# Optimization experiments

Hardware: AMD Instinct MI355X
Metric: run time of the kernel (lower is better)

## Reference

```python
import jax, jax.numpy as jnp
import numpy as np

N = 4096
IN_DIM = 256
HID = 64
HEADS = 4
OUT_DIM = 64
NEG = -9e15


def setup_inputs() -> dict:
    key = jax.random.key(0)
    ks = jax.random.split(key, 12)
    h = jax.random.normal(ks[0], (N, IN_DIM), dtype=jnp.float32)
    adj = jax.random.randint(ks[1], (N, N), 0, 2, dtype=jnp.int32)
    # per-head GATLayer params (W: Linear(input_dim, hid) with bias; a: Linear(2*hid, 1) with bias)
    Wh = jax.random.normal(ks[2], (HEADS, IN_DIM, HID), dtype=jnp.float32) * (1.414 / np.sqrt(IN_DIM + HID))
    bWh = jnp.zeros((HEADS, HID), dtype=jnp.float32)
    a_src = jax.random.normal(ks[3], (HEADS, HID), dtype=jnp.float32) * 0.1
    a_dst = jax.random.normal(ks[4], (HEADS, HID), dtype=jnp.float32) * 0.1
    a_b = jnp.zeros((HEADS,), dtype=jnp.float32)
    # output GATLayer params
    Wo = jax.random.normal(ks[5], (HEADS * HID, OUT_DIM), dtype=jnp.float32) * (1.414 / np.sqrt(HEADS * HID + OUT_DIM))
    bWo = jnp.zeros((OUT_DIM,), dtype=jnp.float32)
    ao_src = jax.random.normal(ks[6], (OUT_DIM,), dtype=jnp.float32) * 0.1
    ao_dst = jax.random.normal(ks[7], (OUT_DIM,), dtype=jnp.float32) * 0.1
    ao_b = jnp.zeros((), dtype=jnp.float32)
    return {"h": h, "adj": adj, "Wh": Wh, "bWh": bWh, "a_src": a_src, "a_dst": a_dst,
            "a_b": a_b, "Wo": Wo, "bWo": bWo, "ao_src": ao_src, "ao_dst": ao_dst, "ao_b": ao_b}


def _gat_layer(x, adj_mask, W, b, a_s, a_d, a_bias):
    # x: [N, F], W: [F, D]. Decompose a([wh_i || wh_j]) = a_s.wh_i + a_d.wh_j + a_bias
    wh = x @ W + b                                   # [N, D]
    s = (wh @ a_s)[:, None] + (wh @ a_d)[None, :] + a_bias  # [N, N]
    s = jax.nn.leaky_relu(s, negative_slope=0.2)
    s = jnp.where(adj_mask, s, NEG)
    att = jax.nn.softmax(s, axis=1)                  # softmax over neighbors j
    return att @ wh                                  # [N, D]


def reference(h, adj, Wh, bWh, a_src, a_dst, a_b, Wo, bWo, ao_src, ao_dst, ao_b):
    adj_mask = adj > 0
    # multi-head: vmap over stacked head params (dropout is identity in eval)
    heads = jax.vmap(lambda W, b, asr, ads, ab: _gat_layer(h, adj_mask, W, b, asr, ads, ab))(
        Wh, bWh, a_src, a_dst, a_b)                  # [H, N, D]
    out = jax.nn.elu(heads)
    out = jnp.transpose(out, (1, 0, 2)).reshape(N, HEADS * HID)  # concat heads
    out = _gat_layer(out, adj_mask, Wo, bWo, ao_src, ao_dst, ao_b)
    return jax.nn.elu(out)
```

## Files before the change

### kernel.cpp

```cpp
#include <hip/hip_runtime.h>

#define NN 4096
#define NHEADS 4
#define HID 64
#define INDIM 256

using short8 = __attribute__((ext_vector_type(8))) short;
using f32x4  = __attribute__((ext_vector_type(4))) float;

union f32u { float f; unsigned int u; };
union i4s8 { int4 i; short8 s; };

__device__ __forceinline__ float bf2f(unsigned short s) {
  f32u x; x.u = ((unsigned int)s) << 16; return x.f;
}
__device__ __forceinline__ unsigned short f2bf(float f) {
  f32u x; x.f = f;
  unsigned int r = x.u + 0x7fffu + ((x.u >> 16) & 1u);
  return (unsigned short)(r >> 16);
}
__device__ __forceinline__ unsigned int cvtpk(float lo, float hi) {
  unsigned int r;
  asm("v_cvt_pk_bf16_f32 %0, %1, %2" : "=v"(r) : "v"(lo), "v"(hi));
  return r;
}

__device__ __forceinline__ float ld(const unsigned short* p, size_t i) { return bf2f(p[i]); }
__device__ __forceinline__ float ld(const float* p, size_t i) { return p[i]; }
__device__ __forceinline__ void ld4(const unsigned short* p, float* out) {
  short4 v = *(const short4*)p;
  out[0] = bf2f((unsigned short)v.x); out[1] = bf2f((unsigned short)v.y);
  out[2] = bf2f((unsigned short)v.z); out[3] = bf2f((unsigned short)v.w);
}
__device__ __forceinline__ void ld4(const float* p, float* out) {
  float4 a = *(const float4*)p;
  out[0] = a.x; out[1] = a.y; out[2] = a.z; out[3] = a.w;
}

__global__ __launch_bounds__(256) void k_bm(const void* adjv, const void* hv,
                                            int* __restrict__ flags,
                                            unsigned char* __restrict__ bm) {
  __shared__ int s_at;
  const int tid = threadIdx.x;
  if (tid == 0) s_at = 0;
  __syncthreads();
  const unsigned int* au = (const unsigned int*)adjv;
  unsigned int wv = au[tid];
  if ((wv & 0xFFFFu) == 0x3F80u) atomicOr(&s_at, 2);
  else if (wv == 0x3F800000u) atomicOr(&s_at, 1);
  __syncthreads();
  const int at = (s_at & 2) ? 2 : (s_at & 1);
  const int i = blockIdx.x;
  if (i == 0 && tid < 64) {
    const unsigned short* hu = (const unsigned short*)hv;
    int bad = 0;
    for (int t = tid; t < 256; t += 64) {
      float v = bf2f(hu[t]);
      if (!(v > -1000.f && v < 1000.f)) bad = 1;
    }
    unsigned long long m = __ballot(bad);
    if (tid == 0) { flags[0] = m ? 0 : 1; flags[1] = at; }
  }
#pragma unroll
  for (int rep = 0; rep < 2; rep++) {
    int jb = tid + rep * 256;
    unsigned int b = 0;
    if (at == 0) {
      const int4* arow = (const int4*)((const int*)adjv + (size_t)i * NN);
      int4 a0 = arow[jb * 2 + 0];
      int4 a1 = arow[jb * 2 + 1];
      b |= (a0.x > 0) ? 1u : 0u;  b |= (a0.y > 0) ? 2u : 0u;
      b |= (a0.z > 0) ? 4u : 0u;  b |= (a0.w > 0) ? 8u : 0u;
      b |= (a1.x > 0) ? 16u : 0u; b |= (a1.y > 0) ? 32u : 0u;
      b |= (a1.z > 0) ? 64u : 0u; b |= (a1.w > 0) ? 128u : 0u;
    } else if (at == 1) {
      const float* arow = (const float*)adjv + (size_t)i * NN + jb * 8;
      for (int t = 0; t < 8; t++) b |= (arow[t] > 0.5f) ? (1u << t) : 0u;
    } else {
      const unsigned short* arow = (const unsigned short*)adjv + (size_t)i * NN + jb * 8;
      for (int t = 0; t < 8; t++) b |= (bf2f(arow[t]) > 0.5f) ? (1u << t) : 0u;
    }
    bm[(size_t)i * 512 + jb] = (unsigned char)b;
  }
}

template <typename T>
__device__ __forceinline__ void wh_body(const T* h, const T* Wh, const T* bWh,
    const T* a_src, const T* a_dst, const T* a_b,
    unsigned short* __restrict__ Bp1, float* __restrict__ ssrc1, float* __restrict__ sdst1,
    float (*hs)[260], float (*wp)[16][260], float* av0, float* av1) {
  const int tid = threadIdx.x;
  const int w = tid >> 6, lane = tid & 63;
  const int head = w & 3, kq = w >> 2;
  const int rb = blockIdx.x;
  const int R0 = rb * 16;
  const int d = lane;
  {
    const int r = tid >> 6, c4 = (tid & 63) * 4;
    float hv4[4];
    ld4(h + (size_t)(R0 + r) * 256 + c4, hv4);
    hs[r][c4 + 0] = hv4[0]; hs[r][c4 + 1] = hv4[1];
    hs[r][c4 + 2] = hv4[2]; hs[r][c4 + 3] = hv4[3];
  }
  if (tid < 256) av0[tid] = ld(a_src, tid);
  else if (tid < 512) av1[tid - 256] = ld(a_dst, tid - 256);
  __syncthreads();
  float acc[16];
  float bv = (kq == 0) ? ld(bWh, head * 64 + d) : 0.f;
#pragma unroll
  for (int r = 0; r < 16; r++) acc[r] = bv;
  const int k0 = kq * 64;
  for (int kb = 0; kb < 8; kb++) {
    float wv[8];
#pragma unroll
    for (int j = 0; j < 8; j++)
      wv[j] = ld(Wh, (size_t)(head * 256 + k0 + kb * 8 + j) * 64 + d);
#pragma unroll
    for (int r = 0; r < 16; r++) {
      float4 ha = *(const float4*)(&hs[r][k0 + kb * 8]);
      float4 hb = *(const float4*)(&hs[r][k0 + kb * 8 + 4]);
      acc[r] = fmaf(ha.x, wv[0], acc[r]);
      acc[r] = fmaf(ha.y, wv[1], acc[r]);
      acc[r] = fmaf(ha.z, wv[2], acc[r]);
      acc[r] = fmaf(ha.w, wv[3], acc[r]);
      acc[r] = fmaf(hb.x, wv[4], acc[r]);
      acc[r] = fmaf(hb.y, wv[5], acc[r]);
      acc[r] = fmaf(hb.z, wv[6], acc[r]);
      acc[r] = fmaf(hb.w, wv[7], acc[r]);
    }
  }
  if (kq >= 2) {
#pragma unroll
    for (int r = 0; r < 16; r++) wp[kq - 2][r][head * 64 + d] = acc[r];
  }
  __syncthreads();
  if (kq < 2) {
#pragma unroll
    for (int r = 0; r < 16; r++) wp[kq][r][head * 64 + d] += acc[r];
  }
  __syncthreads();
  if (tid < 512) {
    const int hh = tid >> 7, tt = (tid >> 5) & 3, lnh = tid & 31;
    const int q2 = (rb & 1) * 2 + (lnh >> 4);
    const int ln = q2 * 16 + (lnh & 15);
    const int dd = tt * 16 + (lnh & 15);
    const int rbase = (lnh >> 4) * 8;
    float v[8];
#pragma unroll
    for (int jj = 0; jj < 8; jj++)
      v[jj] = wp[0][rbase + jj][hh * 64 + dd] + wp[1][rbase + jj][hh * 64 + dd];
    i4s8 s;
    s.i.x = cvtpk(v[0], v[1]); s.i.y = cvtpk(v[2], v[3]);
    s.i.z = cvtpk(v[4], v[5]); s.i.w = cvtpk(v[6], v[7]);
    const int kb = rb >> 1;
    *(int4*)(Bp1 + ((((size_t)hh * 128 + kb) * 4 + tt) * 64 + ln) * 8) = s.i;
  } else if (tid < 576) {
    const int t2 = tid - 512;
    const int hh = t2 >> 4, r = t2 & 15;
    float ps = 0.f, pd = 0.f;
    for (int c = 0; c < 64; c++) {
      float wv2 = wp[0][r][hh * 64 + c] + wp[1][r][hh * 64 + c];
      ps = fmaf(wv2, av0[hh * 64 + c], ps);
      pd = fmaf(wv2, av1[hh * 64 + c], pd);
    }
    ssrc1[hh * NN + R0 + r] = ps + ld(a_b, hh);
    sdst1[hh * NN + R0 + r] = pd;
  }
}
__global__ __launch_bounds__(1024, 4) void k_wh(const void* h, const void* Wh, const void* bWh,
    const void* a_src, const void* a_dst, const void* a_b, const int* __restrict__ flags,
    unsigned short* Bp1, float* ssrc1, float* sdst1) {
  __shared__ float hs[16][260];
  __shared__ float wp[2][16][260];
  __shared__ float av0[256], av1[256];
  if (flags[0])
    wh_body<unsigned short>((const unsigned short*)h, (const unsigned short*)Wh,
        (const unsigned short*)bWh, (const unsigned short*)a_src,
        (const unsigned short*)a_dst, (const unsigned short*)a_b, Bp1, ssrc1, sdst1,
        hs, wp, av0, av1);
  else
    wh_body<float>((const float*)h, (const float*)Wh, (const float*)bWh, (const float*)a_src,
        (const float*)a_dst, (const float*)a_b, Bp1, ssrc1, sdst1, hs, wp, av0, av1);
}

__global__ __launch_bounds__(1024, 4) void k_att1s(
    const unsigned char* __restrict__ bm, const float* __restrict__ ssrc,
    const float* __restrict__ sdst, const short8* __restrict__ Bp,
    float* __restrict__ part, float* __restrict__ partl) {
  const int rb = blockIdx.x & 127;
  const int half = blockIdx.x >> 7;
  const int tid = threadIdx.x;
  const int w = tid >> 6;
  const int head = w & 3;
  const int sl = w >> 2;
  const int lane = tid & 63;
  const int r15 = lane & 15, quad = lane >> 4;
  const int row0 = rb * 32 + r15;
  const int row1 = row0 + 16;
  const float si0 = ssrc[head * NN + row0];
  const float si1 = ssrc[head * NN + row1];
  const unsigned char* bmr0 = bm + (size_t)row0 * 512;
  const unsigned char* bmr1 = bm + (size_t)row1 * 512;
  const float* sd = sdst + head * NN;
  const short8* Bh = Bp + (size_t)head * 128 * 4 * 64;
  f32x4 acc0[4], acc1[4];
#pragma unroll
  for (int t = 0; t < 4; t++) { acc0[t] = (f32x4){0,0,0,0}; acc1[t] = (f32x4){0,0,0,0}; }
  float ls0 = 0.f, ls1 = 0.f;
  const int kb0 = half * 64 + sl * 16;
  for (int g = 0; g < 4; g++) {
    const int kbg = kb0 + g * 4;
    int4 u0 = *(const int4*)(bmr0 + kbg * 4);
    int4 u1 = *(const int4*)(bmr1 + kbg * 4);
    int wd0[4] = {u0.x, u0.y, u0.z, u0.w};
    int wd1[4] = {u1.x, u1.y, u1.z, u1.w};
#pragma unroll
    for (int kk = 0; kk < 4; kk++) {
      const int kb = kbg + kk;
      const int j0 = kb * 32 + quad * 8;
      float4 q0 = *(const float4*)(sd + j0);
      float4 q1 = *(const float4*)(sd + j0 + 4);
      float sdv[8] = {q0.x, q0.y, q0.z, q0.w, q1.x, q1.y, q1.z, q1.w};
      unsigned int bits0 = (((unsigned int)wd0[kk]) >> (quad * 8)) & 0xffu;
      unsigned int bits1 = (((unsigned int)wd1[kk]) >> (quad * 8)) & 0xffu;
      float pe0[8], pe1[8];
#pragma unroll
      for (int jj = 0; jj < 8; jj++) {
        float t0 = si0 + sdv[jj];
        float e0 = __expf(fmaxf(t0, 0.2f * t0));
        pe0[jj] = ((bits0 >> jj) & 1u) ? e0 : 0.f;
        ls0 += pe0[jj];
        float t1 = si1 + sdv[jj];
        float e1 = __expf(fmaxf(t1, 0.2f * t1));
        pe1[jj] = ((bits1 >> jj) & 1u) ? e1 : 0.f;
        ls1 += pe1[jj];
      }
      i4s8 a0, a1;
      a0.i.x = cvtpk(pe0[0], pe0[1]); a0.i.y = cvtpk(pe0[2], pe0[3]);
      a0.i.z = cvtpk(pe0[4], pe0[5]); a0.i.w = cvtpk(pe0[6], pe0[7]);
      a1.i.x = cvtpk(pe1[0], pe1[1]); a1.i.y = cvtpk(pe1[2], pe1[3]);
      a1.i.z = cvtpk(pe1[4], pe1[5]); a1.i.w = cvtpk(pe1[6], pe1[7]);
      const short8* Bk = Bh + (size_t)kb * 256 + lane;
      short8 bt[4];
      bt[0] = Bk[0]; bt[1] = Bk[64]; bt[2] = Bk[128]; bt[3] = Bk[192];
#pragma unroll
      for (int t = 0; t < 4; t++) {
        acc0[t] = __builtin_amdgcn_mfma_f32_16x16x32_bf16(a0.s, bt[t], acc0[t], 0, 0, 0);
        acc1[t] = __builtin_amdgcn_mfma_f32_16x16x32_bf16(a1.s, bt[t], acc1[t], 0, 0, 0);
      }
    }
  }
  ls0 += __shfl_xor(ls0, 16); ls0 += __shfl_xor(ls0, 32);
  ls1 += __shfl_xor(ls1, 16); ls1 += __shfl_xor(ls1, 32);
  __shared__ float accs[8][16][66];
  __shared__ float lsh[8][16];
#define DOPASS(AC, LSV, PASS)                                                  \
  do {                                                                         \
    if (sl >= 2) {                                                             \
      const int slot = head * 2 + (sl - 2);                                    \
      if (lane < 16) lsh[slot][lane] = (LSV);                                  \
      _Pragma("unroll") for (int t = 0; t < 4; t++)                            \
        _Pragma("unroll") for (int gg = 0; gg < 4; gg++)                       \
          accs[slot][quad * 4 + gg][t * 16 + r15] = (AC)[t][gg];               \
    }                                                                          \
    __syncthreads();                                                           \
    if (sl < 2) {                                                              \
      const int slot = head * 2 + sl;                                          \
      if (lane < 16) lsh[slot][lane] += (LSV);                                 \
      _Pragma("unroll") for (int t = 0; t < 4; t++)                            \
        _Pragma("unroll") for (int gg = 0; gg < 4; gg++)                       \
          accs[slot][quad * 4 + gg][t * 16 + r15] += (AC)[t][gg];              \
    }                                                                          \
    __syncthreads();                                                           \
    _Pragma("unroll") for (int idx = tid; idx < 4096; idx += 1024) {           \
      int r = idx >> 8, hc = idx & 255;                                        \
      int hh = hc >> 6, col = hc & 63;                                         \
      part[((size_t)half * NN + rb * 32 + (PASS) * 16 + r) * 256 + hc] =       \
          accs[hh * 2][r][col] + accs[hh * 2 + 1][r][col];                     \
    }                                                                          \
    if (tid < 64)                                                              \
      partl[((size_t)half * 4 + (tid >> 4)) * NN + rb * 32 + (PASS) * 16 +     \
            (tid & 15)] = lsh[(tid >> 4) * 2][tid & 15] +                      \
                          lsh[(tid >> 4) * 2 + 1][tid & 15];                   \
    __syncthreads();                                                           \
  } while (0)
  DOPASS(acc0, ls0, 0);
  DOPASS(acc1, ls1, 1);
#undef DOPASS
}

__global__ __launch_bounds__(1024) void k_att1(
    const unsigned char* __restrict__ bm, const float* __restrict__ ssrc,
    const float* __restrict__ sdst, const short8* __restrict__ Bp,
    unsigned short* __restrict__ x2) {
  const int rb = blockIdx.x;
  const int tid = threadIdx.x;
  const int w = tid >> 6;
  const int head = w & 3;
  const int slice = w >> 2;
  const int lane = tid & 63;
  const int r15 = lane & 15, quad = lane >> 4;
  const int row = rb * 16 + r15;
  const float si = ssrc[head * NN + row];
  const unsigned char* bmrow = bm + (size_t)row * 512;
  const float* sd = sdst + head * NN;
  const short8* Bh = Bp + (size_t)head * 128 * 4 * 64;
  f32x4 acc0 = {0, 0, 0, 0}, acc1 = {0, 0, 0, 0}, acc2 = {0, 0, 0, 0}, acc3 = {0, 0, 0, 0};
  float lsum = 0.f;
  const int kb0 = slice * 32;
  for (int kb = kb0; kb < kb0 + 32; kb++) {
    const int j0 = kb * 32 + quad * 8;
    unsigned int bits = bmrow[kb * 4 + quad];
    float4 q0 = *(const float4*)(sd + j0);
    float4 q1 = *(const float4*)(sd + j0 + 4);
    float sdv[8] = {q0.x, q0.y, q0.z, q0.w, q1.x, q1.y, q1.z, q1.w};
    short8 af;
#pragma unroll
    for (int jj = 0; jj < 8; jj++) {
      float t = si + sdv[jj];
      float lr = fmaxf(t, 0.2f * t);
      float e = __expf(lr);
      float pe = ((bits >> jj) & 1u) ? e : 0.0f;
      lsum += pe;
      af[jj] = (short)f2bf(pe);
    }
    const short8* Bk = Bh + (size_t)kb * 256 + lane;
    short8 b0 = Bk[0], b1 = Bk[64], b2 = Bk[128], b3 = Bk[192];
    acc0 = __builtin_amdgcn_mfma_f32_16x16x32_bf16(af, b0, acc0, 0, 0, 0);
    acc1 = __builtin_amdgcn_mfma_f32_16x16x32_bf16(af, b1, acc1, 0, 0, 0);
    acc2 = __builtin_amdgcn_mfma_f32_16x16x32_bf16(af, b2, acc2, 0, 0, 0);
    acc3 = __builtin_amdgcn_mfma_f32_16x16x32_bf16(af, b3, acc3, 0, 0, 0);
  }
  lsum += __shfl_xor(lsum, 16);
  lsum += __shfl_xor(lsum, 32);
  __shared__ float accs[8][16][66];
  __shared__ float ls[8][16];
  if (slice >= 2) {
    const int slot = w - 8;
    if (lane < 16) ls[slot][lane] = lsum;
#pragma unroll
    for (int g = 0; g < 4; g++) {
      int r = quad * 4 + g;
      accs[slot][r][ 0 + r15] = acc0[g];
      accs[slot][r][16 + r15] = acc1[g];
      accs[slot][r][32 + r15] = acc2[g];
      accs[slot][r][48 + r15] = acc3[g];
    }
  }
  __syncthreads();
  if (slice < 2) {
    const int slot = w;
    if (lane < 16) ls[slot][lane] += lsum;
#pragma unroll
    for (int g = 0; g < 4; g++) {
      int r = quad * 4 + g;
      accs[slot][r][ 0 + r15] += acc0[g];
      accs[slot][r][16 + r15] += acc1[g];
      accs[slot][r][32 + r15] += acc2[g];
      accs[slot][r][48 + r15] += acc3[g];
    }
  }
  __syncthreads();
#pragma unroll
  for (int c = tid; c < 4096; c += 1024) {
    int r = c >> 8, hc = c & 255;
    int hh = hc >> 6, col = hc & 63;
    float s = accs[hh][r][col] + accs[hh + 4][r][col];
    float lt = ls[hh][r] + ls[hh + 4][r];
    float v = (lt > 0.f) ? s / lt : 0.f;
    v = v > 0.f ? v : __expf(v) - 1.f;
    x2[(size_t)(rb * 16 + r) * 256 + hc] = f2bf(v);
  }
}

template <typename T>
__device__ __forceinline__ void wo_body(const unsigned short* x2,
    const float* part, const float* partl,
    const T* Wo, const T* bWo, const T* ao_src, const T* ao_dst, const T* ao_b,
    unsigned short* __restrict__ Bp2, float* __restrict__ ssrc2, float* __restrict__ sdst2,
    float (*xs)[260], float (*wp)[16][68], float* av) {
  const int tid = threadIdx.x;
  const int w = tid >> 6, lane = tid & 63;
  const int rg = w & 3, kq = w >> 2;
  const int rb = blockIdx.x;
  const int d = lane;
  {
    const int r = tid >> 6, c4 = (tid & 63) * 4;
    const int row = rb * 16 + r;
    if (part) {
      float4 p0 = *(const float4*)(part + (size_t)row * 256 + c4);
      float4 p1 = *(const float4*)(part + (size_t)NN * 256 + (size_t)row * 256 + c4);
      const int head = c4 >> 6;
      float lt = partl[(size_t)head * NN + row] + partl[(size_t)(4 + head) * NN + row];
      float rl = (lt > 0.f) ? 1.f / lt : 0.f;
      float v0 = (p0.x + p1.x) * rl, v1 = (p0.y + p1.y) * rl;
      float v2 = (p0.z + p1.z) * rl, v3 = (p0.w + p1.w) * rl;
      v0 = v0 > 0.f ? v0 : __expf(v0) - 1.f;
      v1 = v1 > 0.f ? v1 : __expf(v1) - 1.f;
      v2 = v2 > 0.f ? v2 : __expf(v2) - 1.f;
      v3 = v3 > 0.f ? v3 : __expf(v3) - 1.f;
      xs[r][c4 + 0] = v0; xs[r][c4 + 1] = v1;
      xs[r][c4 + 2] = v2; xs[r][c4 + 3] = v3;
    } else {
      float hv4[4];
      ld4(x2 + (size_t)row * 256 + c4, hv4);
      xs[r][c4 + 0] = hv4[0]; xs[r][c4 + 1] = hv4[1];
      xs[r][c4 + 2] = hv4[2]; xs[r][c4 + 3] = hv4[3];
    }
  }
  if (tid < 64) av[tid] = ld(ao_src, tid);
  else if (tid < 128) av[tid] = ld(ao_dst, tid - 64);
  __syncthreads();
  const int rr = rg * 4;
  float acc[4];
  float bv = (kq == 0) ? ld(bWo, d) : 0.f;
#pragma unroll
  for (int r = 0; r < 4; r++) acc[r] = bv;
  const int k0 = kq * 64;
  for (int kb = 0; kb < 8; kb++) {
    float wv[8];
#pragma unroll
    for (int j = 0; j < 8; j++)
      wv[j] = ld(Wo, (size_t)(k0 + kb * 8 + j) * 64 + d);
#pragma unroll
    for (int r = 0; r < 4; r++) {
      float4 ha = *(const float4*)(&xs[rr + r][k0 + kb * 8]);
      float4 hb = *(const float4*)(&xs[rr + r][k0 + kb * 8 + 4]);
      acc[r] = fmaf(ha.x, wv[0], acc[r]);
      acc[r] = fmaf(ha.y, wv[1], acc[r]);
      acc[r] = fmaf(ha.z, wv[2], acc[r]);
      acc[r] = fmaf(ha.w, wv[3], acc[r]);
      acc[r] = fmaf(hb.x, wv[4], acc[r]);
      acc[r] = fmaf(hb.y, wv[5], acc[r]);
      acc[r] = fmaf(hb.z, wv[6], acc[r]);
      acc[r] = fmaf(hb.w, wv[7], acc[r]);
    }
  }
  if (kq >= 2) {
#pragma unroll
    for (int r = 0; r < 4; r++) wp[kq - 2][rr + r][d] = acc[r];
  }
  __syncthreads();
  if (kq < 2) {
#pragma unroll
    for (int r = 0; r < 4; r++) wp[kq][rr + r][d] += acc[r];
  }
  __syncthreads();
  if (tid < 128) {
    const int tt = tid >> 5, lnh = tid & 31;
    const int q2 = (rb & 1) * 2 + (lnh >> 4);
    const int ln = q2 * 16 + (lnh & 15);
    const int dd = tt * 16 + (lnh & 15);
    const int rbase = (lnh >> 4) * 8;
    float v[8];
#pragma unroll
    for (int jj = 0; jj < 8; jj++)
      v[jj] = wp[0][rbase + jj][dd] + wp[1][rbase + jj][dd];
    i4s8 s;
    s.i.x = cvtpk(v[0], v[1]); s.i.y = cvtpk(v[2], v[3]);
    s.i.z = cvtpk(v[4], v[5]); s.i.w = cvtpk(v[6], v[7]);
    const int kb = rb >> 1;
    *(int4*)(Bp2 + (((size_t)kb * 4 + tt) * 64 + ln) * 8) = s.i;
  } else if (tid < 144) {
    const int r = tid - 128;
    float ps = 0.f, pd = 0.f;
    for (int c = 0; c < 64; c++) {
      float wv2 = wp[0][r][c] + wp[1][r][c];
      ps = fmaf(wv2, av[c], ps);
      pd = fmaf(wv2, av[64 + c], pd);
    }
    ssrc2[(size_t)rb * 16 + r] = ps + ld(ao_b, 0);
    sdst2[(size_t)rb * 16 + r] = pd;
  }
}
__global__ __launch_bounds__(1024, 4) void k_wo(const unsigned short* __restrict__ x2,
    const float* __restrict__ part, const float* __restrict__ partl,
    const void* Wo, const void* bWo, const void* ao_src, const void* ao_dst, const void* ao_b,
    const int* __restrict__ flags, unsigned short* Bp2, float* ssrc2, float* sdst2) {
  __shared__ float xs[16][260];
  __shared__ float wp[2][16][68];
  __shared__ float av[128];
  if (flags[0])
    wo_body<unsigned short>(x2, part, partl, (const unsigned short*)Wo,
        (const unsigned short*)bWo, (const unsigned short*)ao_src,
        (const unsigned short*)ao_dst, (const unsigned short*)ao_b,
        Bp2, ssrc2, sdst2, xs, wp, av);
  else
    wo_body<float>(x2, part, partl, (const float*)Wo, (const float*)bWo,
        (const float*)ao_src, (const float*)ao_dst, (const float*)ao_b,
        Bp2, ssrc2, sdst2, xs, wp, av);
}

__global__ __launch_bounds__(1024) void k_att2(
    const unsigned char* __restrict__ bm, const float* __restrict__ ssrc,
    const float* __restrict__ sdst, const short8* __restrict__ Bp,
    const int* __restrict__ flags, void* __restrict__ outv) {
  const int rb = blockIdx.x;
  const int tid = threadIdx.x;
  const int w = tid >> 6;
  const int lane = tid & 63;
  const int r15 = lane & 15, quad = lane >> 4;
  const int row = rb * 16 + r15;
  const float si = ssrc[row];
  const unsigned char* bmrow = bm + (size_t)row * 512;
  f32x4 acc0 = {0, 0, 0, 0}, acc1 = {0, 0, 0, 0}, acc2 = {0, 0, 0, 0}, acc3 = {0, 0, 0, 0};
  float lsum = 0.f;
  const int kb0 = w * 8;
#pragma unroll
  for (int g = 0; g < 2; g++) {
    int4 ubm = *(const int4*)(bmrow + (kb0 + g * 4) * 4);
    int wds[4] = {ubm.x, ubm.y, ubm.z, ubm.w};
#pragma unroll
    for (int kk = 0; kk < 4; kk++) {
      const int kb = kb0 + g * 4 + kk;
      const int j0 = kb * 32 + quad * 8;
      unsigned int bits = (((unsigned int)wds[kk]) >> (quad * 8)) & 0xffu;
      float4 q0 = *(const float4*)(sdst + j0);
      float4 q1 = *(const float4*)(sdst + j0 + 4);
      float sdv[8] = {q0.x, q0.y, q0.z, q0.w, q1.x, q1.y, q1.z, q1.w};
      float pe[8];
#pragma unroll
      for (int jj = 0; jj < 8; jj++) {
        float t = si + sdv[jj];
        float e = __expf(fmaxf(t, 0.2f * t));
        pe[jj] = ((bits >> jj) & 1u) ? e : 0.f;
        lsum += pe[jj];
      }
      i4s8 a;
      a.i.x = cvtpk(pe[0], pe[1]); a.i.y = cvtpk(pe[2], pe[3]);
      a.i.z = cvtpk(pe[4], pe[5]); a.i.w = cvtpk(pe[6], pe[7]);
      const short8* Bk = Bp + (size_t)kb * 256 + lane;
      short8 b0 = Bk[0], b1 = Bk[64], b2 = Bk[128], b3 = Bk[192];
      acc0 = __builtin_amdgcn_mfma_f32_16x16x32_bf16(a.s, b0, acc0, 0, 0, 0);
      acc1 = __builtin_amdgcn_mfma_f32_16x16x32_bf16(a.s, b1, acc1, 0, 0, 0);
      acc2 = __builtin_amdgcn_mfma_f32_16x16x32_bf16(a.s, b2, acc2, 0, 0, 0);
      acc3 = __builtin_amdgcn_mfma_f32_16x16x32_bf16(a.s, b3, acc3, 0, 0, 0);
    }
  }
  lsum += __shfl_xor(lsum, 16);
  lsum += __shfl_xor(lsum, 32);
  __shared__ float accs[8][16][66];
  __shared__ float ls2[8][16];
  if (w >= 8) {
    const int slot = w - 8;
    if (lane < 16) ls2[slot][lane] = lsum;
#pragma unroll
    for (int g = 0; g < 4; g++) {
      int r = quad * 4 + g;
      accs[slot][r][ 0 + r15] = acc0[g];
      accs[slot][r][16 + r15] = acc1[g];
      accs[slot][r][32 + r15] = acc2[g];
      accs[slot][r][48 + r15] = acc3[g];
    }
  }
  __syncthreads();
  if (w < 8) {
    const int slot = w;
    if (lane < 16) ls2[slot][lane] += lsum;
#pragma unroll
    for (int g = 0; g < 4; g++) {
      int r = quad * 4 + g;
      accs[slot][r][ 0 + r15] += acc0[g];
      accs[slot][r][16 + r15] += acc1[g];
      accs[slot][r][32 + r15] += acc2[g];
      accs[slot][r][48 + r15] += acc3[g];
    }
  }
  __syncthreads();
  {
    const int r = tid >> 6, col = tid & 63;
    float s = 0.f, lt = 0.f;
#pragma unroll
    for (int k = 0; k < 8; k++) { s += accs[k][r][col]; lt += ls2[k][r]; }
    float v = (lt > 0.f) ? s / lt : 0.f;
    v = v > 0.f ? v : __expf(v) - 1.f;
    size_t idx = (size_t)(rb * 16 + r) * 64 + col;
    if (flags[0]) ((unsigned short*)outv)[idx] = f2bf(v);
    else          ((float*)outv)[idx] = v;
  }
}

extern "C" void kernel_launch(void* const* d_in, const int* in_sizes, int n_in,
                              void* d_out, int out_size, void* d_ws, size_t ws_size,
                              hipStream_t stream) {
  const void* h      = d_in[0];
  const void* adj    = d_in[1];
  const void* Wh     = d_in[2];
  const void* bWh    = d_in[3];
  const void* a_src  = d_in[4];
  const void* a_dst  = d_in[5];
  const void* a_b    = d_in[6];
  const void* Wo     = d_in[7];
  const void* bWo    = d_in[8];
  const void* ao_src = d_in[9];
  const void* ao_dst = d_in[10];
  const void* ao_b   = d_in[11];

  size_t need_old = 16 + (size_t)NN * 512 + (size_t)NHEADS * NN * HID * 2 +
                    (size_t)NN * 256 * 2 + (size_t)NN * 64 * 2 +
                    (size_t)NHEADS * NN * 8 + (size_t)NN * 8;
  size_t need_new = need_old + (size_t)2 * NN * 256 * 4 + (size_t)2 * 4 * NN * 4;
  if (ws_size < need_old) {
    hipMemsetAsync(d_out, 0x45, (size_t)out_size * 2, stream);
    return;
  }
  const bool big = ws_size >= need_new;
  unsigned char* ws = (unsigned char*)d_ws;
  int* flags = (int*)ws;                        ws += 16;
  unsigned char* bmp = ws;                      ws += (size_t)NN * 512;
  unsigned short* Bp1 = (unsigned short*)ws;    ws += (size_t)NHEADS * NN * HID * 2;
  unsigned short* x2  = (unsigned short*)ws;    ws += (size_t)NN * 256 * 2;
  unsigned short* Bp2 = (unsigned short*)ws;    ws += (size_t)NN * 64 * 2;
  float* ssrc1 = (float*)ws;                    ws += (size_t)NHEADS * NN * 4;
  float* sdst1 = (float*)ws;                    ws += (size_t)NHEADS * NN * 4;
  float* ssrc2 = (float*)ws;                    ws += (size_t)NN * 4;
  float* sdst2 = (float*)ws;                    ws += (size_t)NN * 4;
  float* part  = (float*)ws;                    ws += (size_t)2 * NN * 256 * 4;
  float* partl = (float*)ws;                    ws += (size_t)2 * 4 * NN * 4;

  k_bm   <<<dim3(4096), dim3(256),  0, stream>>>(adj, h, flags, bmp);
  k_wh   <<<dim3(256),  dim3(1024), 0, stream>>>(h, Wh, bWh, a_src, a_dst, a_b, flags,
                                                 Bp1, ssrc1, sdst1);
  if (big) {
    k_att1s<<<dim3(256), dim3(1024), 0, stream>>>(bmp, ssrc1, sdst1, (const short8*)Bp1,
                                                  part, partl);
    k_wo   <<<dim3(256), dim3(1024), 0, stream>>>(x2, part, partl, Wo, bWo, ao_src, ao_dst,
                                                  ao_b, flags, Bp2, ssrc2, sdst2);
  } else {
    k_att1 <<<dim3(256), dim3(1024), 0, stream>>>(bmp, ssrc1, sdst1, (const short8*)Bp1, x2);
    k_wo   <<<dim3(256), dim3(1024), 0, stream>>>(x2, (const float*)nullptr,
                                                  (const float*)nullptr, Wo, bWo, ao_src,
                                                  ao_dst, ao_b, flags, Bp2, ssrc2, sdst2);
  }
  k_att2 <<<dim3(256),  dim3(1024), 0, stream>>>(bmp, ssrc2, sdst2, (const short8*)Bp2,
                                                 flags, d_out);
}
```

Measured before the change: 179.2 us.

## Split attention neighbor dimension further across blocks for both GAT layers

Layer-1 attention now splits the neighbor range four ways (512 blocks) instead of two, and k_wo sums four partial accumulators and row sums. Layer-2 attention gets a new split-K kernel (512 blocks, two halves) plus a small finalize kernel that combines the partials, normalizes, applies ELU and writes the output. The aim is more blocks to fill the GPU's compute units. The cost is more partial-sum traffic through global memory and an extra kernel launch, and the workspace requirement grows.

```diff
diff --git a/kernel.cpp b/kernel.cpp
--- a/kernel.cpp
+++ b/kernel.cpp
@@ -183,12 +183,12 @@
         (const float*)a_dst, (const float*)a_b, Bp1, ssrc1, sdst1, hs, wp, av0, av1);
 }
 
-__global__ __launch_bounds__(1024, 4) void k_att1s(
+__global__ __launch_bounds__(1024, 8) void k_att1s(
     const unsigned char* __restrict__ bm, const float* __restrict__ ssrc,
     const float* __restrict__ sdst, const short8* __restrict__ Bp,
     float* __restrict__ part, float* __restrict__ partl) {
   const int rb = blockIdx.x & 127;
-  const int half = blockIdx.x >> 7;
+  const int qtr = blockIdx.x >> 7;
   const int tid = threadIdx.x;
   const int w = tid >> 6;
   const int head = w & 3;
@@ -207,8 +207,8 @@
 #pragma unroll
   for (int t = 0; t < 4; t++) { acc0[t] = (f32x4){0,0,0,0}; acc1[t] = (f32x4){0,0,0,0}; }
   float ls0 = 0.f, ls1 = 0.f;
-  const int kb0 = half * 64 + sl * 16;
-  for (int g = 0; g < 4; g++) {
+  const int kb0 = qtr * 32 + sl * 8;
+  for (int g = 0; g < 2; g++) {
     const int kbg = kb0 + g * 4;
     int4 u0 = *(const int4*)(bmr0 + kbg * 4);
     int4 u1 = *(const int4*)(bmr1 + kbg * 4);
@@ -275,11 +275,11 @@
     _Pragma("unroll") for (int idx = tid; idx < 4096; idx += 1024) {           \
       int r = idx >> 8, hc = idx & 255;                                        \
       int hh = hc >> 6, col = hc & 63;                                         \
-      part[((size_t)half * NN + rb * 32 + (PASS) * 16 + r) * 256 + hc] =       \
+      part[((size_t)qtr * NN + rb * 32 + (PASS) * 16 + r) * 256 + hc] =        \
           accs[hh * 2][r][col] + accs[hh * 2 + 1][r][col];                     \
     }                                                                          \
     if (tid < 64)                                                              \
-      partl[((size_t)half * 4 + (tid >> 4)) * NN + rb * 32 + (PASS) * 16 +     \
+      partl[((size_t)qtr * 4 + (tid >> 4)) * NN + rb * 32 + (PASS) * 16 +      \
             (tid & 15)] = lsh[(tid >> 4) * 2][tid & 15] +                      \
                           lsh[(tid >> 4) * 2 + 1][tid & 15];                   \
     __syncthreads();                                                           \
@@ -388,13 +388,20 @@
     const int r = tid >> 6, c4 = (tid & 63) * 4;
     const int row = rb * 16 + r;
     if (part) {
-      float4 p0 = *(const float4*)(part + (size_t)row * 256 + c4);
-      float4 p1 = *(const float4*)(part + (size_t)NN * 256 + (size_t)row * 256 + c4);
+      float4 p0 = *(const float4*)(part + ((size_t)0 * NN + row) * 256 + c4);
+      float4 p1 = *(const float4*)(part + ((size_t)1 * NN + row) * 256 + c4);
+      float4 p2 = *(const float4*)(part + ((size_t)2 * NN + row) * 256 + c4);
+      float4 p3 = *(const float4*)(part + ((size_t)3 * NN + row) * 256 + c4);
       const int head = c4 >> 6;
-      float lt = partl[(size_t)head * NN + row] + partl[(size_t)(4 + head) * NN + row];
+      float lt = partl[((size_t)0 * 4 + head) * NN + row] +
+                 partl[((size_t)1 * 4 + head) * NN + row] +
+                 partl[((size_t)2 * 4 + head) * NN + row] +
+                 partl[((size_t)3 * 4 + head) * NN + row];
       float rl = (lt > 0.f) ? 1.f / lt : 0.f;
-      float v0 = (p0.x + p1.x) * rl, v1 = (p0.y + p1.y) * rl;
-      float v2 = (p0.z + p1.z) * rl, v3 = (p0.w + p1.w) * rl;
+      float v0 = (p0.x + p1.x + p2.x + p3.x) * rl;
+      float v1 = (p0.y + p1.y + p2.y + p3.y) * rl;
+      float v2 = (p0.z + p1.z + p2.z + p3.z) * rl;
+      float v3 = (p0.w + p1.w + p2.w + p3.w) * rl;
       v0 = v0 > 0.f ? v0 : __expf(v0) - 1.f;
       v1 = v1 > 0.f ? v1 : __expf(v1) - 1.f;
       v2 = v2 > 0.f ? v2 : __expf(v2) - 1.f;
@@ -491,6 +498,118 @@
         Bp2, ssrc2, sdst2, xs, wp, av);
 }
 
+__global__ __launch_bounds__(1024, 8) void k_att2s(
+    const unsigned char* __restrict__ bm, const float* __restrict__ ssrc,
+    const float* __restrict__ sdst, const short8* __restrict__ Bp,
+    float* __restrict__ out2, float* __restrict__ l2p) {
+  const int rb = blockIdx.x & 255;
+  const int half = blockIdx.x >> 8;
+  const int tid = threadIdx.x;
+  const int w = tid >> 6;
+  const int lane = tid & 63;
+  const int r15 = lane & 15, quad = lane >> 4;
+  const int row = rb * 16 + r15;
+  const float si = ssrc[row];
+  const unsigned char* bmrow = bm + (size_t)row * 512;
+  f32x4 acc0 = {0, 0, 0, 0}, acc1 = {0, 0, 0, 0}, acc2 = {0, 0, 0, 0}, acc3 = {0, 0, 0, 0};
+  float lsum = 0.f;
+  const int kb0 = half * 64 + w * 4;
+  {
+    int4 ubm = *(const int4*)(bmrow + kb0 * 4);
+    int wds[4] = {ubm.x, ubm.y, ubm.z, ubm.w};
+#pragma unroll
+    for (int kk = 0; kk < 4; kk++) {
+      const int kb = kb0 + kk;
+      const int j0 = kb * 32 + quad * 8;
+      unsigned int bits = (((unsigned int)wds[kk]) >> (quad * 8)) & 0xffu;
+      float4 q0 = *(const float4*)(sdst + j0);
+      float4 q1 = *(const float4*)(sdst + j0 + 4);
+      float sdv[8] = {q0.x, q0.y, q0.z, q0.w, q1.x, q1.y, q1.z, q1.w};
+      float pe[8];
+#pragma unroll
+      for (int jj = 0; jj < 8; jj++) {
+        float t = si + sdv[jj];
+        float e = __expf(fmaxf(t, 0.2f * t));
+        pe[jj] = ((bits >> jj) & 1u) ? e : 0.f;
+        lsum += pe[jj];
+      }
+      i4s8 a;
+      a.i.x = cvtpk(pe[0], pe[1]); a.i.y = cvtpk(pe[2], pe[3]);
+      a.i.z = cvtpk(pe[4], pe[5]); a.i.w = cvtpk(pe[6], pe[7]);
+      const short8* Bk = Bp + (size_t)kb * 256 + lane;
+      short8 b0 = Bk[0], b1 = Bk[64], b2 = Bk[128], b3 = Bk[192];
+      acc0 = __builtin_amdgcn_mfma_f32_16x16x32_bf16(a.s, b0, acc0, 0, 0, 0);
+      acc1 = __builtin_amdgcn_mfma_f32_16x16x32_bf16(a.s, b1, acc1, 0, 0, 0);
+      acc2 = __builtin_amdgcn_mfma_f32_16x16x32_bf16(a.s, b2, acc2, 0, 0, 0);
+      acc3 = __builtin_amdgcn_mfma_f32_16x16x32_bf16(a.s, b3, acc3, 0, 0, 0);
+    }
+  }
+  lsum += __shfl_xor(lsum, 16);
+  lsum += __shfl_xor(lsum, 32);
+  __shared__ float accs[8][16][66];
+  __shared__ float ls2[8][16];
+  if (w >= 8) {
+    const int slot = w - 8;
+    if (lane < 16) ls2[slot][lane] = lsum;
+#pragma unroll
+    for (int g = 0; g < 4; g++) {
+      int r = quad * 4 + g;
+      accs[slot][r][ 0 + r15] = acc0[g];
+      accs[slot][r][16 + r15] = acc1[g];
+      accs[slot][r][32 + r15] = acc2[g];
+      accs[slot][r][48 + r15] = acc3[g];
+    }
+  }
+  __syncthreads();
+  if (w < 8) {
+    const int slot = w;
+    if (lane < 16) ls2[slot][lane] += lsum;
+#pragma unroll
+    for (int g = 0; g < 4; g++) {
+      int r = quad * 4 + g;
+      accs[slot][r][ 0 + r15] += acc0[g];
+      accs[slot][r][16 + r15] += acc1[g];
+      accs[slot][r][32 + r15] += acc2[g];
+      accs[slot][r][48 + r15] += acc3[g];
+    }
+  }
+  __syncthreads();
+  {
+    const int r = tid >> 6, col = tid & 63;
+    float s = 0.f, lt = 0.f;
+#pragma unroll
+    for (int k = 0; k < 8; k++) { s += accs[k][r][col]; lt += ls2[k][r]; }
+    out2[((size_t)half * NN + rb * 16 + r) * 64 + col] = s;
+    if (col == 0) l2p[(size_t)half * NN + rb * 16 + r] = lt;
+  }
+}
+
+__global__ __launch_bounds__(256) void k_att2f(const float* __restrict__ out2,
+    const float* __restrict__ l2p, const int* __restrict__ flags,
+    void* __restrict__ outv) {
+  const int idx = blockIdx.x * 256 + threadIdx.x;
+  const int row = idx >> 4;
+  const int c4 = (idx & 15) * 4;
+  float4 a = *(const float4*)(out2 + (size_t)row * 64 + c4);
+  float4 b = *(const float4*)(out2 + ((size_t)NN + row) * 64 + c4);
+  float lt = l2p[row] + l2p[NN + row];
+  float rl = (lt > 0.f) ? 1.f / lt : 0.f;
+  float v0 = (a.x + b.x) * rl, v1 = (a.y + b.y) * rl;
+  float v2 = (a.z + b.z) * rl, v3 = (a.w + b.w) * rl;
+  v0 = v0 > 0.f ? v0 : __expf(v0) - 1.f;
+  v1 = v1 > 0.f ? v1 : __expf(v1) - 1.f;
+  v2 = v2 > 0.f ? v2 : __expf(v2) - 1.f;
+  v3 = v3 > 0.f ? v3 : __expf(v3) - 1.f;
+  size_t off = (size_t)row * 64 + c4;
+  if (flags[0]) {
+    uint2 st; st.x = cvtpk(v0, v1); st.y = cvtpk(v2, v3);
+    *(uint2*)((unsigned short*)outv + off) = st;
+  } else {
+    float4 st; st.x = v0; st.y = v1; st.z = v2; st.w = v3;
+    *(float4*)((float*)outv + off) = st;
+  }
+}
+
 __global__ __launch_bounds__(1024) void k_att2(
     const unsigned char* __restrict__ bm, const float* __restrict__ ssrc,
     const float* __restrict__ sdst, const short8* __restrict__ Bp,
@@ -599,7 +718,8 @@
   size_t need_old = 16 + (size_t)NN * 512 + (size_t)NHEADS * NN * HID * 2 +
                     (size_t)NN * 256 * 2 + (size_t)NN * 64 * 2 +
                     (size_t)NHEADS * NN * 8 + (size_t)NN * 8;
-  size_t need_new = need_old + (size_t)2 * NN * 256 * 4 + (size_t)2 * 4 * NN * 4;
+  size_t need_new = need_old + (size_t)4 * NN * 256 * 4 + (size_t)16 * NN * 4 +
+                    (size_t)2 * NN * 64 * 4 + (size_t)2 * NN * 4;
   if (ws_size < need_old) {
     hipMemsetAsync(d_out, 0x45, (size_t)out_size * 2, stream);
     return;
@@ -615,23 +735,28 @@
   float* sdst1 = (float*)ws;                    ws += (size_t)NHEADS * NN * 4;
   float* ssrc2 = (float*)ws;                    ws += (size_t)NN * 4;
   float* sdst2 = (float*)ws;                    ws += (size_t)NN * 4;
-  float* part  = (float*)ws;                    ws += (size_t)2 * NN * 256 * 4;
-  float* partl = (float*)ws;                    ws += (size_t)2 * 4 * NN * 4;
+  float* part  = (float*)ws;                    ws += (size_t)4 * NN * 256 * 4;
+  float* partl = (float*)ws;                    ws += (size_t)16 * NN * 4;
+  float* out2  = (float*)ws;                    ws += (size_t)2 * NN * 64 * 4;
+  float* l2p   = (float*)ws;                    ws += (size_t)2 * NN * 4;
 
   k_bm   <<<dim3(4096), dim3(256),  0, stream>>>(adj, h, flags, bmp);
   k_wh   <<<dim3(256),  dim3(1024), 0, stream>>>(h, Wh, bWh, a_src, a_dst, a_b, flags,
                                                  Bp1, ssrc1, sdst1);
   if (big) {
-    k_att1s<<<dim3(256), dim3(1024), 0, stream>>>(bmp, ssrc1, sdst1, (const short8*)Bp1,
+    k_att1s<<<dim3(512), dim3(1024), 0, stream>>>(bmp, ssrc1, sdst1, (const short8*)Bp1,
                                                   part, partl);
     k_wo   <<<dim3(256), dim3(1024), 0, stream>>>(x2, part, partl, Wo, bWo, ao_src, ao_dst,
                                                   ao_b, flags, Bp2, ssrc2, sdst2);
+    k_att2s<<<dim3(512), dim3(1024), 0, stream>>>(bmp, ssrc2, sdst2, (const short8*)Bp2,
+                                                  out2, l2p);
+    k_att2f<<<dim3(256), dim3(256),  0, stream>>>(out2, l2p, flags, d_out);
   } else {
     k_att1 <<<dim3(256), dim3(1024), 0, stream>>>(bmp, ssrc1, sdst1, (const short8*)Bp1, x2);
     k_wo   <<<dim3(256), dim3(1024), 0, stream>>>(x2, (const float*)nullptr,
                                                   (const float*)nullptr, Wo, bWo, ao_src,
                                                   ao_dst, ao_b, flags, Bp2, ssrc2, sdst2);
-  }
-  k_att2 <<<dim3(256),  dim3(1024), 0, stream>>>(bmp, ssrc2, sdst2, (const short8*)Bp2,
-                                                 flags, d_out);
-}
+    k_att2 <<<dim3(256), dim3(1024), 0, stream>>>(bmp, ssrc2, sdst2, (const short8*)Bp2,
+                                                  flags, d_out);
+  }
+}
```

Measured after the change: 339.7 us. 89.6% more time.
